# Performance work log

Measured on AMD Instinct MI355X. Metric: run time of the kernel, lower is better.

## Reference

```python
import jax, jax.numpy as jnp
import numpy as np

E = 8           # num experts
T = 8192        # total tokens
K = 4096        # input dim
N = 4096        # output dim


def setup_inputs() -> dict:
    key = jax.random.key(0)
    k1, k2, k3 = jax.random.split(key, 3)
    a = jax.random.normal(k1, (T, K), dtype=jnp.float32)
    b = jax.random.normal(k2, (E, N, K), dtype=jnp.float32) * 0.02  # column-major expert weights
    c = jnp.zeros((T, N), dtype=jnp.float32)
    inner = jnp.sort(jax.random.randint(k3, (E - 1,), 0, T))
    seg_indptr = jnp.concatenate([jnp.zeros((1,), jnp.int64),
                                  inner.astype(jnp.int64),
                                  jnp.full((1,), T, jnp.int64)])
    weight_indices = jnp.arange(E, dtype=jnp.int64)
    return {"a": a, "b": b, "c": c, "seg_indptr": seg_indptr,
            "weight_indices": weight_indices, "batch_size": E}


def reference(a, b, c, seg_indptr, weight_indices, batch_size):
    # Grouped GEMM: tokens in segment [seg_indptr[e], seg_indptr[e+1]) use
    # expert weight b[weight_indices[e]] (column-major: out = a @ W.T).
    t = a.shape[0]
    b_sel = b[weight_indices]                                  # [E, N, K]
    out_all = jnp.einsum('tk,enk->etn', a, b_sel)              # [E, T, N]
    tok = jnp.arange(t)
    # expert id of each token from sorted segment boundaries
    eid = jnp.clip(jnp.searchsorted(seg_indptr, tok, side='right') - 1,
                   0, batch_size - 1)
    return out_all[eid, tok]                                   # [T, N]
```

## Files before the change

kernel.cpp:

```cpp
#include <hip/hip_runtime.h>
#include <hip/hip_bf16.h>

typedef float f32x4 __attribute__((ext_vector_type(4)));
typedef short bf16x8 __attribute__((ext_vector_type(8)));
typedef unsigned short u16;

constexpr int T_TOK = 8192;
constexpr int KDIM  = 4096;
constexpr int NDIM  = 4096;
constexpr int NE    = 8;

constexpr long long TA = (long long)T_TOK * KDIM;
constexpr long long TB = (long long)NE * NDIM * KDIM;

__device__ __forceinline__ u16 f2bf(float f) {
  unsigned u = __builtin_bit_cast(unsigned, f);
  u += 0x7FFFu + ((u >> 16) & 1u);
  return (u16)(u >> 16);
}

__global__ __launch_bounds__(256)
void cvt_bf16(const float* __restrict__ A, const float* __restrict__ B,
              u16* __restrict__ oA, u16* __restrict__ oB) {
  const long long nv = (TA + TB) >> 3;
  const long long stride = (long long)gridDim.x * blockDim.x;
  for (long long i = (long long)blockIdx.x * blockDim.x + threadIdx.x; i < nv; i += stride) {
    const long long e = i << 3;
    const float* s;
    u16* d;
    if (e < TA) { s = A + e;        d = oA + e; }
    else        { s = B + (e - TA); d = oB + (e - TA); }
    f32x4 v0 = ((const f32x4*)s)[0];
    f32x4 v1 = ((const f32x4*)s)[1];
    bf16x8 p;
    #pragma unroll
    for (int j = 0; j < 4; ++j) p[j]     = (short)f2bf(v0[j]);
    #pragma unroll
    for (int j = 0; j < 4; ++j) p[4 + j] = (short)f2bf(v1[j]);
    *(bf16x8*)d = p;
  }
}

__device__ __forceinline__ void gload16(const u16* g, const u16* l) {
  __builtin_amdgcn_global_load_lds(
      (const __attribute__((address_space(1))) void*)g,
      (__attribute__((address_space(3))) void*)l, 16, 0, 0);
}

constexpr int BM2 = 256, BN2 = 256, BK2 = 64;
constexpr int NKT2 = KDIM / BK2;
constexpr int NTN2 = NDIM / BN2;
constexpr int MT2  = T_TOK / BM2 + NE;
constexpr int NWG2 = MT2 * NTN2;
constexpr int ASZ  = BM2 * BK2;
constexpr int HSZ  = ASZ / 2;

__global__ __launch_bounds__(512, 2)
void gg8(const u16* __restrict__ Abf, const u16* __restrict__ Bbf,
         float* __restrict__ C, const int* __restrict__ segp,
         const int* __restrict__ widx)
{
  extern __shared__ u16 sm[];
  u16* sA = sm;
  u16* sB = sm + 2 * ASZ;

  int bid = (int)blockIdx.x;
  bid = (bid & 7) * (NWG2 / 8) + (bid >> 3);
  const int nt = bid % NTN2;
  const int mt = bid / NTN2;

  int e = -1, segs = 0, sege = 0, mloc = 0;
  {
    int acc0 = 0, sp = segp[0];
    #pragma unroll
    for (int i = 0; i < NE; ++i) {
      int sn = segp[i + 1];
      int nti = (sn - sp + BM2 - 1) / BM2;
      if (e < 0 && mt < acc0 + nti) { e = i; mloc = mt - acc0; segs = sp; sege = sn; }
      acc0 += nti; sp = sn;
    }
  }
  if (e < 0) return;

  const int row_base = segs + mloc * BM2;
  const int col_base = nt * BN2;
  const u16* __restrict__ W = Bbf + (long long)widx[e] * ((long long)NDIM * KDIM);

  const int tid = threadIdx.x, lane = tid & 63, wid = tid >> 6;
  const int wr = wid >> 2, wc = wid & 3;

  const int sg = (((lane & 7) ^ (lane >> 3)) << 3);
  const int rr = wid * 8 + (lane >> 3);
  int oA[2][2], oB[2][2];
  #pragma unroll
  for (int h = 0; h < 2; ++h)
    #pragma unroll
    for (int i = 0; i < 2; ++i) {
      oA[h][i] = min(row_base + h * 128 + i * 64 + rr, T_TOK - 1) * KDIM + sg;
      oB[h][i] = (col_base + h * 128 + i * 64 + rr) * KDIM + sg;
    }

  const int g0  = (lane >> 4) ^ (lane & 7);
  const int g1  = g0 ^ 4;
  const int rA0 = (wr * 64 + (lane & 15)) * BK2 + g0 * 8;
  const int rA1 = (wr * 64 + (lane & 15)) * BK2 + g1 * 8;
  const int rB0 = (wc * 32 + (lane & 15)) * BK2 + g0 * 8;
  const int rB1 = (wc * 32 + (lane & 15)) * BK2 + g1 * 8;

  f32x4 acc[8][4];
  #pragma unroll
  for (int m = 0; m < 8; ++m)
    #pragma unroll
    for (int n = 0; n < 4; ++n)
      acc[m][n] = (f32x4){0.f, 0.f, 0.f, 0.f};

  bf16x8 aF[4][2], bF0[2][2], bF1[2][2];

  auto STGA = [&](int bbuf, int h, int t) __attribute__((always_inline)) {
    gload16(Abf + oA[h][0] + t * BK2, sA + bbuf * ASZ + h * HSZ + wid * 512);
    gload16(Abf + oA[h][1] + t * BK2, sA + bbuf * ASZ + h * HSZ + 4096 + wid * 512);
  };
  auto STGB = [&](int bbuf, int h, int t) __attribute__((always_inline)) {
    gload16(W + oB[h][0] + t * BK2, sB + bbuf * ASZ + h * HSZ + wid * 512);
    gload16(W + oB[h][1] + t * BK2, sB + bbuf * ASZ + h * HSZ + 4096 + wid * 512);
  };
  auto LDA = [&](int bbuf, int mh) __attribute__((always_inline)) {
    #pragma unroll
    for (int j = 0; j < 4; ++j) {
      const u16* p = sA + bbuf * ASZ + mh * HSZ + j * 16 * BK2;
      aF[j][0] = *(const bf16x8*)(p + rA0);
      aF[j][1] = *(const bf16x8*)(p + rA1);
    }
  };
  auto LDB = [&](int bbuf, int nh, bf16x8 (&bF)[2][2]) __attribute__((always_inline)) {
    #pragma unroll
    for (int i = 0; i < 2; ++i) {
      const u16* p = sB + bbuf * ASZ + nh * HSZ + i * 16 * BK2;
      bF[i][0] = *(const bf16x8*)(p + rB0);
      bF[i][1] = *(const bf16x8*)(p + rB1);
    }
  };
  auto MF = [&](int mh, int nh, bf16x8 (&bF)[2][2]) __attribute__((always_inline)) {
    __builtin_amdgcn_s_setprio(1);
    #pragma unroll
    for (int j = 0; j < 4; ++j)
      #pragma unroll
      for (int i = 0; i < 2; ++i) {
        acc[mh * 4 + j][nh * 2 + i] = __builtin_amdgcn_mfma_f32_16x16x32_bf16(
            aF[j][0], bF[i][0], acc[mh * 4 + j][nh * 2 + i], 0, 0, 0);
        acc[mh * 4 + j][nh * 2 + i] = __builtin_amdgcn_mfma_f32_16x16x32_bf16(
            aF[j][1], bF[i][1], acc[mh * 4 + j][nh * 2 + i], 0, 0, 0);
      }
    __builtin_amdgcn_s_setprio(0);
  };

  STGA(0, 0, 0); STGB(0, 0, 0); STGA(0, 1, 0); STGB(0, 1, 0);
  STGA(1, 0, 1); STGB(1, 0, 1);
  asm volatile("s_waitcnt vmcnt(4)" ::: "memory");
  __builtin_amdgcn_s_barrier();

  for (int t = 0; t < NKT2; ++t) {
    const int bb = t & 1, nb = bb ^ 1;

    LDA(bb, 0); LDB(bb, 0, bF0); LDB(bb, 1, bF1);
    if (t + 1 < NKT2) { STGA(nb, 1, t + 1); STGB(nb, 1, t + 1); }
    MF(0, 0, bF0); MF(0, 1, bF1);
    __builtin_amdgcn_s_barrier();

    LDA(bb, 1);
    if (t + 2 < NKT2) { STGA(bb, 0, t + 2); STGB(bb, 0, t + 2); }
    MF(1, 0, bF0); MF(1, 1, bF1);
    if (t + 2 < NKT2) {
      asm volatile("s_waitcnt vmcnt(4)" ::: "memory");
    } else {
      asm volatile("s_waitcnt vmcnt(0)" ::: "memory");
    }
    __builtin_amdgcn_s_barrier();
  }

  #pragma unroll
  for (int m = 0; m < 8; ++m) {
    const int r0 = row_base + (m >> 2) * 128 + wr * 64 + (m & 3) * 16 + ((lane >> 4) << 2);
    #pragma unroll
    for (int j = 0; j < 4; ++j) {
      const int r = r0 + j;
      if (r < sege) {
        float* cp = C + (long long)r * NDIM + col_base + (lane & 15);
        #pragma unroll
        for (int n = 0; n < 4; ++n)
          cp[(n >> 1) * 128 + wc * 32 + (n & 1) * 16] = acc[m][n][j];
      }
    }
  }
}

constexpr int BM = 128, BN = 128, BK = 32;
constexpr int LDKF = BK + 8;
constexpr int NTN = NDIM / BN;
constexpr int MT_MAX = T_TOK / BM + NE;
constexpr int NKT = KDIM / BK;
constexpr int NWG = MT_MAX * NTN;

__global__ __launch_bounds__(256, 2)
void grouped_gemm_fused(const float* __restrict__ A, const float* __restrict__ B,
                        float* __restrict__ C, const int* __restrict__ segp,
                        const int* __restrict__ widx)
{
  __shared__ u16 lA[2][BM][LDKF];
  __shared__ u16 lB[2][BN][LDKF];

  const int nt = blockIdx.x % NTN;
  const int mt = blockIdx.x / NTN;

  int e = -1, segs = 0, sege = 0, mloc = 0;
  {
    int acc0 = 0, sp = segp[0];
    #pragma unroll
    for (int i = 0; i < NE; ++i) {
      int sn = segp[i + 1];
      int nti = (sn - sp + BM - 1) / BM;
      if (e < 0 && mt < acc0 + nti) { e = i; mloc = mt - acc0; segs = sp; sege = sn; }
      acc0 += nti; sp = sn;
    }
  }
  if (e < 0) return;

  const int row_base = segs + mloc * BM;
  const int col_base = nt * BN;
  const float* __restrict__ W = B + (long long)widx[e] * NDIM * KDIM;

  const int tid  = threadIdx.x;
  const int lane = tid & 63;
  const int wid  = tid >> 6;
  const int wr   = wid >> 1;
  const int wc   = wid & 1;

  const int srow = tid >> 1;
  const int scol = (tid & 1) << 4;
  const int arow = min(row_base + srow, T_TOK - 1);
  const float* __restrict__ aptr = A + (long long)arow * KDIM + scol;
  const float* __restrict__ bptr = W + (long long)(col_base + srow) * KDIM + scol;

  f32x4 sa[4], sb[4];
  f32x4 acc[4][4];
  #pragma unroll
  for (int m = 0; m < 4; ++m)
    #pragma unroll
    for (int n = 0; n < 4; ++n)
      acc[m][n] = (f32x4){0.f, 0.f, 0.f, 0.f};

  const int frow = lane & 15;
  const int fk   = (lane >> 4) << 3;

  auto load_tiles = [&](int kt) {
    const float* ap = aptr + kt * BK;
    const float* bp = bptr + kt * BK;
    #pragma unroll
    for (int i = 0; i < 4; ++i) sa[i] = *(const f32x4*)(ap + i * 4);
    #pragma unroll
    for (int i = 0; i < 4; ++i) sb[i] = *(const f32x4*)(bp + i * 4);
  };
  auto conv_write = [&](int buf) {
    u16* wa = &lA[buf][srow][scol];
    u16* wb = &lB[buf][srow][scol];
    bf16x8 p;
    #pragma unroll
    for (int j = 0; j < 8; ++j) p[j] = (short)f2bf(sa[j >> 2][j & 3]);
    *(bf16x8*)(wa) = p;
    #pragma unroll
    for (int j = 0; j < 8; ++j) p[j] = (short)f2bf(sa[2 + (j >> 2)][j & 3]);
    *(bf16x8*)(wa + 8) = p;
    #pragma unroll
    for (int j = 0; j < 8; ++j) p[j] = (short)f2bf(sb[j >> 2][j & 3]);
    *(bf16x8*)(wb) = p;
    #pragma unroll
    for (int j = 0; j < 8; ++j) p[j] = (short)f2bf(sb[2 + (j >> 2)][j & 3]);
    *(bf16x8*)(wb + 8) = p;
  };

  load_tiles(0);
  conv_write(0);
  __syncthreads();

  int cur = 0;
  for (int kt = 0; kt < NKT; ++kt) {
    const bool more = (kt + 1 < NKT);
    if (more) load_tiles(kt + 1);

    bf16x8 af[4], bfr[4];
    #pragma unroll
    for (int m = 0; m < 4; ++m)
      af[m] = *(const bf16x8*)&lA[cur][wr * 64 + m * 16 + frow][fk];
    #pragma unroll
    for (int n = 0; n < 4; ++n)
      bfr[n] = *(const bf16x8*)&lB[cur][wc * 64 + n * 16 + frow][fk];

    if (more) conv_write(cur ^ 1);

    #pragma unroll
    for (int m = 0; m < 4; ++m)
      #pragma unroll
      for (int n = 0; n < 4; ++n)
        acc[m][n] = __builtin_amdgcn_mfma_f32_16x16x32_bf16(af[m], bfr[n], acc[m][n], 0, 0, 0);

    __syncthreads();
    cur ^= 1;
  }

  const int crow0 = row_base + wr * 64;
  const int ccol  = col_base + wc * 64 + (lane & 15);
  const int rsub  = (lane >> 4) << 2;
  #pragma unroll
  for (int m = 0; m < 4; ++m) {
    #pragma unroll
    for (int j = 0; j < 4; ++j) {
      const int r = crow0 + m * 16 + rsub + j;
      if (r < sege) {
        #pragma unroll
        for (int n = 0; n < 4; ++n)
          C[(long long)r * NDIM + ccol + n * 16] = acc[m][n][j];
      }
    }
  }
}

extern "C" void kernel_launch(void* const* d_in, const int* in_sizes, int n_in,
                              void* d_out, int out_size, void* d_ws, size_t ws_size,
                              hipStream_t stream) {
  const float* A   = (const float*)d_in[0];
  const float* B   = (const float*)d_in[1];
  const int* segp  = (const int*)d_in[3];
  const int* widx  = (const int*)d_in[4];
  float* C = (float*)d_out;

  const size_t need = (size_t)(TA + TB) * sizeof(u16);
  if (ws_size >= need) {
    u16* oA = (u16*)d_ws;
    u16* oB = oA + TA;
    cvt_bf16<<<dim3(2048), dim3(256), 0, stream>>>(A, B, oA, oB);
    (void)hipFuncSetAttribute((const void*)gg8,
                              hipFuncAttributeMaxDynamicSharedMemorySize,
                              2 * 2 * ASZ * (int)sizeof(u16));
    gg8<<<dim3(NWG2), dim3(512), 2 * 2 * ASZ * sizeof(u16), stream>>>(oA, oB, C, segp, widx);
  } else {
    grouped_gemm_fused<<<dim3(NWG), dim3(256), 0, stream>>>(A, B, C, segp, widx);
  }
}
```

Baseline: 492.1 us.

## Shrink bf16 grouped GEMM tile to 128x256x32 and simplify the pipeline

Replaces the 256x256x64 tile with a 128x256 tile and BK=32, and launch bounds now ask for 4 workgroups per CU instead of 2. The split-half LDS staging and interleaved MFMA schedule is replaced by a simpler loop: read all fragments, barrier, issue the next stage, then run 16 MFMAs. Per-workgroup LDS and registers drop, which should raise occupancy and cut padding waste on the last tile of each expert segment. In exchange, arithmetic intensity per tile is lower, there are more K iterations with barriers, and global traffic per flop rises.

```diff
diff --git a/kernel.cpp b/kernel.cpp
--- a/kernel.cpp
+++ b/kernel.cpp
@@ -47,27 +47,28 @@
       (__attribute__((address_space(3))) void*)l, 16, 0, 0);
 }
 
-constexpr int BM2 = 256, BN2 = 256, BK2 = 64;
-constexpr int NKT2 = KDIM / BK2;
-constexpr int NTN2 = NDIM / BN2;
-constexpr int MT2  = T_TOK / BM2 + NE;
-constexpr int NWG2 = MT2 * NTN2;
-constexpr int ASZ  = BM2 * BK2;
-constexpr int HSZ  = ASZ / 2;
-
-__global__ __launch_bounds__(512, 2)
+constexpr int BM3 = 128, BN3 = 256, BK3 = 32;
+constexpr int NKT3 = KDIM / BK3;
+constexpr int NTN3 = NDIM / BN3;
+constexpr int MT3  = T_TOK / BM3 + NE;
+constexpr int NWG3 = MT3 * NTN3;
+constexpr int ASZA = BM3 * BK3;
+constexpr int ASZB = BN3 * BK3;
+constexpr int LDS_BYTES = 2 * (ASZA + ASZB) * (int)sizeof(u16);
+
+__global__ __launch_bounds__(512, 4)
 void gg8(const u16* __restrict__ Abf, const u16* __restrict__ Bbf,
          float* __restrict__ C, const int* __restrict__ segp,
          const int* __restrict__ widx)
 {
   extern __shared__ u16 sm[];
   u16* sA = sm;
-  u16* sB = sm + 2 * ASZ;
+  u16* sB = sm + 2 * ASZA;
 
   int bid = (int)blockIdx.x;
-  bid = (bid & 7) * (NWG2 / 8) + (bid >> 3);
-  const int nt = bid % NTN2;
-  const int mt = bid / NTN2;
+  bid = (bid & 7) * (NWG3 / 8) + (bid >> 3);
+  const int nt = bid % NTN3;
+  const int mt = bid / NTN3;
 
   int e = -1, segs = 0, sege = 0, mloc = 0;
   {
@@ -75,103 +76,76 @@
     #pragma unroll
     for (int i = 0; i < NE; ++i) {
       int sn = segp[i + 1];
-      int nti = (sn - sp + BM2 - 1) / BM2;
+      int nti = (sn - sp + BM3 - 1) / BM3;
       if (e < 0 && mt < acc0 + nti) { e = i; mloc = mt - acc0; segs = sp; sege = sn; }
       acc0 += nti; sp = sn;
     }
   }
   if (e < 0) return;
 
-  const int row_base = segs + mloc * BM2;
-  const int col_base = nt * BN2;
+  const int row_base = segs + mloc * BM3;
+  const int col_base = nt * BN3;
   const u16* __restrict__ W = Bbf + (long long)widx[e] * ((long long)NDIM * KDIM);
 
   const int tid = threadIdx.x, lane = tid & 63, wid = tid >> 6;
   const int wr = wid >> 2, wc = wid & 3;
 
-  const int sg = (((lane & 7) ^ (lane >> 3)) << 3);
-  const int rr = wid * 8 + (lane >> 3);
-  int oA[2][2], oB[2][2];
+  const int sgc = ((lane & 3) ^ ((lane >> 3) & 3)) * 8;
+  int oA, oB0, oB1;
+  {
+    const int ra = row_base + wid * 16 + (lane >> 2);
+    oA  = min(ra, T_TOK - 1) * KDIM + sgc;
+    oB0 = (col_base + wid * 32 +      (lane >> 2)) * KDIM + sgc;
+    oB1 = (col_base + wid * 32 + 16 + (lane >> 2)) * KDIM + sgc;
+  }
+
+  const int gp  = ((lane >> 4) ^ ((lane >> 1) & 3)) * 8;
+  const int rA0 = (wr * 64 + (lane & 15)) * BK3 + gp;
+  const int rB0 = (wc * 64 + (lane & 15)) * BK3 + gp;
+
+  f32x4 acc[4][4];
   #pragma unroll
-  for (int h = 0; h < 2; ++h)
-    #pragma unroll
-    for (int i = 0; i < 2; ++i) {
-      oA[h][i] = min(row_base + h * 128 + i * 64 + rr, T_TOK - 1) * KDIM + sg;
-      oB[h][i] = (col_base + h * 128 + i * 64 + rr) * KDIM + sg;
-    }
-
-  const int g0  = (lane >> 4) ^ (lane & 7);
-  const int g1  = g0 ^ 4;
-  const int rA0 = (wr * 64 + (lane & 15)) * BK2 + g0 * 8;
-  const int rA1 = (wr * 64 + (lane & 15)) * BK2 + g1 * 8;
-  const int rB0 = (wc * 32 + (lane & 15)) * BK2 + g0 * 8;
-  const int rB1 = (wc * 32 + (lane & 15)) * BK2 + g1 * 8;
-
-  f32x4 acc[8][4];
-  #pragma unroll
-  for (int m = 0; m < 8; ++m)
+  for (int m = 0; m < 4; ++m)
     #pragma unroll
     for (int n = 0; n < 4; ++n)
       acc[m][n] = (f32x4){0.f, 0.f, 0.f, 0.f};
 
-  bf16x8 aF[4][2], bF0[2][2], bF1[2][2];
-
-  auto STGA = [&](int bbuf, int h, int t) __attribute__((always_inline)) {
-    gload16(Abf + oA[h][0] + t * BK2, sA + bbuf * ASZ + h * HSZ + wid * 512);
-    gload16(Abf + oA[h][1] + t * BK2, sA + bbuf * ASZ + h * HSZ + 4096 + wid * 512);
+  auto STAGE = [&](int bbuf, int t) __attribute__((always_inline)) {
+    gload16(Abf + oA  + t * BK3, sA + bbuf * ASZA + wid * 512);
+    gload16(W   + oB0 + t * BK3, sB + bbuf * ASZB + wid * 1024);
+    gload16(W   + oB1 + t * BK3, sB + bbuf * ASZB + wid * 1024 + 512);
   };
-  auto STGB = [&](int bbuf, int h, int t) __attribute__((always_inline)) {
-    gload16(W + oB[h][0] + t * BK2, sB + bbuf * ASZ + h * HSZ + wid * 512);
-    gload16(W + oB[h][1] + t * BK2, sB + bbuf * ASZ + h * HSZ + 4096 + wid * 512);
-  };
-  auto LDA = [&](int bbuf, int mh) __attribute__((always_inline)) {
-    #pragma unroll
-    for (int j = 0; j < 4; ++j) {
-      const u16* p = sA + bbuf * ASZ + mh * HSZ + j * 16 * BK2;
-      aF[j][0] = *(const bf16x8*)(p + rA0);
-      aF[j][1] = *(const bf16x8*)(p + rA1);
-    }
-  };
-  auto LDB = [&](int bbuf, int nh, bf16x8 (&bF)[2][2]) __attribute__((always_inline)) {
-    #pragma unroll
-    for (int i = 0; i < 2; ++i) {
-      const u16* p = sB + bbuf * ASZ + nh * HSZ + i * 16 * BK2;
-      bF[i][0] = *(const bf16x8*)(p + rB0);
-      bF[i][1] = *(const bf16x8*)(p + rB1);
-    }
-  };
-  auto MF = [&](int mh, int nh, bf16x8 (&bF)[2][2]) __attribute__((always_inline)) {
+
+  STAGE(0, 0); STAGE(1, 1);
+  asm volatile("s_waitcnt vmcnt(3)" ::: "memory");
+  __builtin_amdgcn_s_barrier();
+
+  for (int t = 0; t < NKT3; ++t) {
+    const int bb = t & 1;
+
+    bf16x8 aF[4], bF[4];
+    #pragma unroll
+    for (int m = 0; m < 4; ++m)
+      aF[m] = *(const bf16x8*)(sA + bb * ASZA + rA0 + m * 512);
+    #pragma unroll
+    for (int n = 0; n < 4; ++n)
+      bF[n] = *(const bf16x8*)(sB + bb * ASZB + rB0 + n * 512);
+
+    asm volatile("s_waitcnt lgkmcnt(0)" ::: "memory");
+    __builtin_amdgcn_s_barrier();
+
+    if (t + 2 < NKT3) STAGE(bb, t + 2);
+
     __builtin_amdgcn_s_setprio(1);
     #pragma unroll
-    for (int j = 0; j < 4; ++j)
+    for (int m = 0; m < 4; ++m)
       #pragma unroll
-      for (int i = 0; i < 2; ++i) {
-        acc[mh * 4 + j][nh * 2 + i] = __builtin_amdgcn_mfma_f32_16x16x32_bf16(
-            aF[j][0], bF[i][0], acc[mh * 4 + j][nh * 2 + i], 0, 0, 0);
-        acc[mh * 4 + j][nh * 2 + i] = __builtin_amdgcn_mfma_f32_16x16x32_bf16(
-            aF[j][1], bF[i][1], acc[mh * 4 + j][nh * 2 + i], 0, 0, 0);
-      }
+      for (int n = 0; n < 4; ++n)
+        acc[m][n] = __builtin_amdgcn_mfma_f32_16x16x32_bf16(aF[m], bF[n], acc[m][n], 0, 0, 0);
     __builtin_amdgcn_s_setprio(0);
-  };
-
-  STGA(0, 0, 0); STGB(0, 0, 0); STGA(0, 1, 0); STGB(0, 1, 0);
-  STGA(1, 0, 1); STGB(1, 0, 1);
-  asm volatile("s_waitcnt vmcnt(4)" ::: "memory");
-  __builtin_amdgcn_s_barrier();
-
-  for (int t = 0; t < NKT2; ++t) {
-    const int bb = t & 1, nb = bb ^ 1;
-
-    LDA(bb, 0); LDB(bb, 0, bF0); LDB(bb, 1, bF1);
-    if (t + 1 < NKT2) { STGA(nb, 1, t + 1); STGB(nb, 1, t + 1); }
-    MF(0, 0, bF0); MF(0, 1, bF1);
-    __builtin_amdgcn_s_barrier();
-
-    LDA(bb, 1);
-    if (t + 2 < NKT2) { STGA(bb, 0, t + 2); STGB(bb, 0, t + 2); }
-    MF(1, 0, bF0); MF(1, 1, bF1);
-    if (t + 2 < NKT2) {
-      asm volatile("s_waitcnt vmcnt(4)" ::: "memory");
+
+    if (t + 2 < NKT3) {
+      asm volatile("s_waitcnt vmcnt(3)" ::: "memory");
     } else {
       asm volatile("s_waitcnt vmcnt(0)" ::: "memory");
     }
@@ -179,16 +153,16 @@
   }
 
   #pragma unroll
-  for (int m = 0; m < 8; ++m) {
-    const int r0 = row_base + (m >> 2) * 128 + wr * 64 + (m & 3) * 16 + ((lane >> 4) << 2);
+  for (int m = 0; m < 4; ++m) {
+    const int r0 = row_base + wr * 64 + m * 16 + ((lane >> 4) << 2);
     #pragma unroll
     for (int j = 0; j < 4; ++j) {
       const int r = r0 + j;
       if (r < sege) {
-        float* cp = C + (long long)r * NDIM + col_base + (lane & 15);
+        float* cp = C + (long long)r * NDIM + col_base + wc * 64 + (lane & 15);
         #pragma unroll
         for (int n = 0; n < 4; ++n)
-          cp[(n >> 1) * 128 + wc * 32 + (n & 1) * 16] = acc[m][n][j];
+          cp[n * 16] = acc[m][n][j];
       }
     }
   }
@@ -340,8 +314,8 @@
     cvt_bf16<<<dim3(2048), dim3(256), 0, stream>>>(A, B, oA, oB);
     (void)hipFuncSetAttribute((const void*)gg8,
                               hipFuncAttributeMaxDynamicSharedMemorySize,
-                              2 * 2 * ASZ * (int)sizeof(u16));
-    gg8<<<dim3(NWG2), dim3(512), 2 * 2 * ASZ * sizeof(u16), stream>>>(oA, oB, C, segp, widx);
+                              LDS_BYTES);
+    gg8<<<dim3(NWG3), dim3(512), LDS_BYTES, stream>>>(oA, oB, C, segp, widx);
   } else {
     grouped_gemm_fused<<<dim3(NWG), dim3(256), 0, stream>>>(A, B, C, segp, widx);
   }
```

Measured after the change: 568.2 us. +15.5%, slower.

## Switch grouped GEMM inner loop to 32x32x16 bf16 MFMA with new LDS swizzle

Applied to the files above, without the earlier changes.

Replaces the 16x16x32 MFMA tiling with 32x32x16 MFMA instructions. Each wave now owns a 64-column strip made of two 32x32 fragments in N and two in M per half. The LDS write swizzle gains an extra XOR by wave index, and the read pattern changes to match the 32-lane fragment layout. The aim is fewer LDS fragment reads per FLOP and higher MFMA throughput per instruction. In exchange it rewrites the epilogue mapping and risks bank conflicts or a mismatch between the write and read swizzles.

```diff
diff --git a/kernel.cpp b/kernel.cpp
--- a/kernel.cpp
+++ b/kernel.cpp
@@ -2,6 +2,7 @@
 #include <hip/hip_bf16.h>
 
 typedef float f32x4 __attribute__((ext_vector_type(4)));
+typedef float f32x16 __attribute__((ext_vector_type(16)));
 typedef short bf16x8 __attribute__((ext_vector_type(8)));
 typedef unsigned short u16;
 
@@ -89,7 +90,7 @@
   const int tid = threadIdx.x, lane = tid & 63, wid = tid >> 6;
   const int wr = wid >> 2, wc = wid & 3;
 
-  const int sg = (((lane & 7) ^ (lane >> 3)) << 3);
+  const int sg = (((lane & 7) ^ ((lane >> 3) & 7) ^ (wid & 3)) << 3);
   const int rr = wid * 8 + (lane >> 3);
   int oA[2][2], oB[2][2];
   #pragma unroll
@@ -100,21 +101,23 @@
       oB[h][i] = (col_base + h * 128 + i * 64 + rr) * KDIM + sg;
     }
 
-  const int g0  = (lane >> 4) ^ (lane & 7);
-  const int g1  = g0 ^ 4;
-  const int rA0 = (wr * 64 + (lane & 15)) * BK2 + g0 * 8;
-  const int rA1 = (wr * 64 + (lane & 15)) * BK2 + g1 * 8;
-  const int rB0 = (wc * 32 + (lane & 15)) * BK2 + g0 * 8;
-  const int rB1 = (wc * 32 + (lane & 15)) * BK2 + g1 * 8;
-
-  f32x4 acc[8][4];
-  #pragma unroll
-  for (int m = 0; m < 8; ++m)
-    #pragma unroll
-    for (int n = 0; n < 4; ++n)
-      acc[m][n] = (f32x4){0.f, 0.f, 0.f, 0.f};
-
-  bf16x8 aF[4][2], bF0[2][2], bF1[2][2];
+  const int klane = (lane & 7) ^ ((lane >> 3) & 3);
+  int pgk[4];
+  #pragma unroll
+  for (int ks = 0; ks < 4; ++ks)
+    pgk[ks] = ((ks * 2 + (lane >> 5)) ^ klane) * 8;
+  const int rAin = (wr * 64 + (lane & 31)) * BK2;
+  const int rBin = ((wc & 1) * 64 + (lane & 31)) * BK2;
+  const int hB   = wc >> 1;
+
+  f32x16 acc[2][2][2];
+  #pragma unroll
+  for (int a = 0; a < 2; ++a)
+    #pragma unroll
+    for (int b = 0; b < 2; ++b)
+      #pragma unroll
+      for (int c = 0; c < 2; ++c)
+        acc[a][b][c] = (f32x16)(0.f);
 
   auto STGA = [&](int bbuf, int h, int t) __attribute__((always_inline)) {
     gload16(Abf + oA[h][0] + t * BK2, sA + bbuf * ASZ + h * HSZ + wid * 512);
@@ -124,52 +127,55 @@
     gload16(W + oB[h][0] + t * BK2, sB + bbuf * ASZ + h * HSZ + wid * 512);
     gload16(W + oB[h][1] + t * BK2, sB + bbuf * ASZ + h * HSZ + 4096 + wid * 512);
   };
-  auto LDA = [&](int bbuf, int mh) __attribute__((always_inline)) {
-    #pragma unroll
-    for (int j = 0; j < 4; ++j) {
-      const u16* p = sA + bbuf * ASZ + mh * HSZ + j * 16 * BK2;
-      aF[j][0] = *(const bf16x8*)(p + rA0);
-      aF[j][1] = *(const bf16x8*)(p + rA1);
-    }
-  };
-  auto LDB = [&](int bbuf, int nh, bf16x8 (&bF)[2][2]) __attribute__((always_inline)) {
-    #pragma unroll
-    for (int i = 0; i < 2; ++i) {
-      const u16* p = sB + bbuf * ASZ + nh * HSZ + i * 16 * BK2;
-      bF[i][0] = *(const bf16x8*)(p + rB0);
-      bF[i][1] = *(const bf16x8*)(p + rB1);
-    }
-  };
-  auto MF = [&](int mh, int nh, bf16x8 (&bF)[2][2]) __attribute__((always_inline)) {
-    __builtin_amdgcn_s_setprio(1);
-    #pragma unroll
-    for (int j = 0; j < 4; ++j)
-      #pragma unroll
-      for (int i = 0; i < 2; ++i) {
-        acc[mh * 4 + j][nh * 2 + i] = __builtin_amdgcn_mfma_f32_16x16x32_bf16(
-            aF[j][0], bF[i][0], acc[mh * 4 + j][nh * 2 + i], 0, 0, 0);
-        acc[mh * 4 + j][nh * 2 + i] = __builtin_amdgcn_mfma_f32_16x16x32_bf16(
-            aF[j][1], bF[i][1], acc[mh * 4 + j][nh * 2 + i], 0, 0, 0);
-      }
-    __builtin_amdgcn_s_setprio(0);
-  };
 
   STGA(0, 0, 0); STGB(0, 0, 0); STGA(0, 1, 0); STGB(0, 1, 0);
   STGA(1, 0, 1); STGB(1, 0, 1);
   asm volatile("s_waitcnt vmcnt(4)" ::: "memory");
   __builtin_amdgcn_s_barrier();
 
+  bf16x8 aF[2][4], bF[2][4];
   for (int t = 0; t < NKT2; ++t) {
     const int bb = t & 1, nb = bb ^ 1;
 
-    LDA(bb, 0); LDB(bb, 0, bF0); LDB(bb, 1, bF1);
+    #pragma unroll
+    for (int nf = 0; nf < 2; ++nf)
+      #pragma unroll
+      for (int ks = 0; ks < 4; ++ks)
+        bF[nf][ks] = *(const bf16x8*)(sB + bb * ASZ + hB * HSZ + rBin + nf * 2048 + pgk[ks]);
+    #pragma unroll
+    for (int mf = 0; mf < 2; ++mf)
+      #pragma unroll
+      for (int ks = 0; ks < 4; ++ks)
+        aF[mf][ks] = *(const bf16x8*)(sA + bb * ASZ + rAin + mf * 2048 + pgk[ks]);
     if (t + 1 < NKT2) { STGA(nb, 1, t + 1); STGB(nb, 1, t + 1); }
-    MF(0, 0, bF0); MF(0, 1, bF1);
+    __builtin_amdgcn_s_setprio(1);
+    #pragma unroll
+    for (int ks = 0; ks < 4; ++ks)
+      #pragma unroll
+      for (int mf = 0; mf < 2; ++mf)
+        #pragma unroll
+        for (int nf = 0; nf < 2; ++nf)
+          acc[0][mf][nf] = __builtin_amdgcn_mfma_f32_32x32x16_bf16(
+              aF[mf][ks], bF[nf][ks], acc[0][mf][nf], 0, 0, 0);
+    __builtin_amdgcn_s_setprio(0);
     __builtin_amdgcn_s_barrier();
 
-    LDA(bb, 1);
+    #pragma unroll
+    for (int mf = 0; mf < 2; ++mf)
+      #pragma unroll
+      for (int ks = 0; ks < 4; ++ks)
+        aF[mf][ks] = *(const bf16x8*)(sA + bb * ASZ + HSZ + rAin + mf * 2048 + pgk[ks]);
     if (t + 2 < NKT2) { STGA(bb, 0, t + 2); STGB(bb, 0, t + 2); }
-    MF(1, 0, bF0); MF(1, 1, bF1);
+    __builtin_amdgcn_s_setprio(1);
+    #pragma unroll
+    for (int ks = 0; ks < 4; ++ks)
+      #pragma unroll
+      for (int mf = 0; mf < 2; ++mf)
+        #pragma unroll
+        for (int nf = 0; nf < 2; ++nf)
+          acc[1][mf][nf] = __builtin_amdgcn_mfma_f32_32x32x16_bf16(
+              aF[mf][ks], bF[nf][ks], acc[1][mf][nf], 0, 0, 0);
+    __builtin_amdgcn_s_setprio(0);
     if (t + 2 < NKT2) {
       asm volatile("s_waitcnt vmcnt(4)" ::: "memory");
     } else {
@@ -178,20 +184,24 @@
     __builtin_amdgcn_s_barrier();
   }
 
-  #pragma unroll
-  for (int m = 0; m < 8; ++m) {
-    const int r0 = row_base + (m >> 2) * 128 + wr * 64 + (m & 3) * 16 + ((lane >> 4) << 2);
-    #pragma unroll
-    for (int j = 0; j < 4; ++j) {
-      const int r = r0 + j;
-      if (r < sege) {
-        float* cp = C + (long long)r * NDIM + col_base + (lane & 15);
+  const int ccol = col_base + wc * 64 + (lane & 31);
+  #pragma unroll
+  for (int mh = 0; mh < 2; ++mh)
+    #pragma unroll
+    for (int mf = 0; mf < 2; ++mf) {
+      const int r0 = row_base + mh * 128 + wr * 64 + mf * 32 + ((lane >> 5) << 2);
+      #pragma unroll
+      for (int rq = 0; rq < 4; ++rq)
         #pragma unroll
-        for (int n = 0; n < 4; ++n)
-          cp[(n >> 1) * 128 + wc * 32 + (n & 1) * 16] = acc[m][n][j];
-      }
-    }
-  }
+        for (int rj = 0; rj < 4; ++rj) {
+          const int r = r0 + rq * 8 + rj;
+          if (r < sege) {
+            float* cp = C + (long long)r * NDIM + ccol;
+            cp[0]  = acc[mh][mf][0][rq * 4 + rj];
+            cp[32] = acc[mh][mf][1][rq * 4 + rj];
+          }
+        }
+    }
 }
 
 constexpr int BM = 128, BN = 128, BK = 32;
```

After: 539.1 us. +9.5%, slower.

## Split grouped GEMM into full-tile wave plus half-height tail kernel

Applied to the files above, without the earlier changes.

The first 512 256x256 tiles (one full wave at two workgroups per CU) now run in the original kernel. The remaining tail tiles go to a new kernel that splits each tile into two 128x256 halves, so twice as many workgroups share the tail work across CUs. The goal is to shrink the underfilled last wave and the imbalance it causes. The cost is a second kernel launch with a serialization point between the two, lower per-block reuse in the half tiles, and possibly wasted work on half tiles that fall past a segment end. Tile decoding is factored into a shared helper.

```diff
diff --git a/kernel.cpp b/kernel.cpp
--- a/kernel.cpp
+++ b/kernel.cpp
@@ -51,9 +51,24 @@
 constexpr int NKT2 = KDIM / BK2;
 constexpr int NTN2 = NDIM / BN2;
 constexpr int MT2  = T_TOK / BM2 + NE;
-constexpr int NWG2 = MT2 * NTN2;
+constexpr int NWG_TOT = MT2 * NTN2;
+constexpr int NWG_L1  = 512;
 constexpr int ASZ  = BM2 * BK2;
 constexpr int HSZ  = ASZ / 2;
+
+__device__ __forceinline__ bool decode_tile(const int* segp, int mt,
+                                            int& e, int& segs, int& sege, int& mloc) {
+  e = -1;
+  int acc0 = 0, sp = segp[0];
+  #pragma unroll
+  for (int i = 0; i < NE; ++i) {
+    int sn = segp[i + 1];
+    int nti = (sn - sp + BM2 - 1) / BM2;
+    if (e < 0 && mt < acc0 + nti) { e = i; mloc = mt - acc0; segs = sp; sege = sn; }
+    acc0 += nti; sp = sn;
+  }
+  return e >= 0;
+}
 
 __global__ __launch_bounds__(512, 2)
 void gg8(const u16* __restrict__ Abf, const u16* __restrict__ Bbf,
@@ -65,22 +80,12 @@
   u16* sB = sm + 2 * ASZ;
 
   int bid = (int)blockIdx.x;
-  bid = (bid & 7) * (NWG2 / 8) + (bid >> 3);
+  bid = (bid & 7) * (NWG_L1 / 8) + (bid >> 3);
   const int nt = bid % NTN2;
   const int mt = bid / NTN2;
 
-  int e = -1, segs = 0, sege = 0, mloc = 0;
-  {
-    int acc0 = 0, sp = segp[0];
-    #pragma unroll
-    for (int i = 0; i < NE; ++i) {
-      int sn = segp[i + 1];
-      int nti = (sn - sp + BM2 - 1) / BM2;
-      if (e < 0 && mt < acc0 + nti) { e = i; mloc = mt - acc0; segs = sp; sege = sn; }
-      acc0 += nti; sp = sn;
-    }
-  }
-  if (e < 0) return;
+  int e, segs, sege, mloc;
+  if (!decode_tile(segp, mt, e, segs, sege, mloc)) return;
 
   const int row_base = segs + mloc * BM2;
   const int col_base = nt * BN2;
@@ -194,6 +199,124 @@
   }
 }
 
+__global__ __launch_bounds__(512, 2)
+void gg_half(const u16* __restrict__ Abf, const u16* __restrict__ Bbf,
+             float* __restrict__ C, const int* __restrict__ segp,
+             const int* __restrict__ widx)
+{
+  extern __shared__ u16 sm[];
+  u16* sA = sm;
+  u16* sB = sm + 2 * HSZ;
+
+  int b = (int)blockIdx.x;
+  const int swz = (b & 7) * 32 + (b >> 3);
+  const int tile = NWG_L1 + (swz >> 1);
+  const int mh   = swz & 1;
+  const int nt = tile % NTN2;
+  const int mt = tile / NTN2;
+
+  int e, segs, sege, mloc;
+  if (!decode_tile(segp, mt, e, segs, sege, mloc)) return;
+
+  const int row_base = segs + mloc * BM2 + mh * 128;
+  const int col_base = nt * BN2;
+  const u16* __restrict__ W = Bbf + (long long)widx[e] * ((long long)NDIM * KDIM);
+
+  const int tid = threadIdx.x, lane = tid & 63, wid = tid >> 6;
+  const int wr = wid >> 2, wc = wid & 3;
+
+  const int sg = (((lane & 7) ^ (lane >> 3)) << 3);
+  const int rr = wid * 8 + (lane >> 3);
+  int oA[2], oB[4];
+  #pragma unroll
+  for (int i = 0; i < 2; ++i)
+    oA[i] = min(row_base + i * 64 + rr, T_TOK - 1) * KDIM + sg;
+  #pragma unroll
+  for (int i = 0; i < 4; ++i)
+    oB[i] = (col_base + i * 64 + rr) * KDIM + sg;
+
+  const int g0  = (lane >> 4) ^ (lane & 7);
+  const int g1  = g0 ^ 4;
+  const int rA0 = (wr * 64 + (lane & 15)) * BK2 + g0 * 8;
+  const int rA1 = (wr * 64 + (lane & 15)) * BK2 + g1 * 8;
+  const int rB0 = (wc * 64 + (lane & 15)) * BK2 + g0 * 8;
+  const int rB1 = (wc * 64 + (lane & 15)) * BK2 + g1 * 8;
+
+  f32x4 acc[4][4];
+  #pragma unroll
+  for (int m = 0; m < 4; ++m)
+    #pragma unroll
+    for (int n = 0; n < 4; ++n)
+      acc[m][n] = (f32x4){0.f, 0.f, 0.f, 0.f};
+
+  auto STAGE = [&](int bbuf, int t) __attribute__((always_inline)) {
+    gload16(Abf + oA[0] + t * BK2, sA + bbuf * HSZ + wid * 512);
+    gload16(Abf + oA[1] + t * BK2, sA + bbuf * HSZ + 4096 + wid * 512);
+    #pragma unroll
+    for (int i = 0; i < 4; ++i)
+      gload16(W + oB[i] + t * BK2, sB + bbuf * ASZ + i * 4096 + wid * 512);
+  };
+
+  STAGE(0, 0); STAGE(1, 1);
+  asm volatile("s_waitcnt vmcnt(6)" ::: "memory");
+  __builtin_amdgcn_s_barrier();
+
+  for (int t = 0; t < NKT2; ++t) {
+    const int bb = t & 1;
+
+    bf16x8 aF[4][2], bF[4][2];
+    #pragma unroll
+    for (int m = 0; m < 4; ++m) {
+      const u16* p = sA + bb * HSZ + m * 16 * BK2;
+      aF[m][0] = *(const bf16x8*)(p + rA0);
+      aF[m][1] = *(const bf16x8*)(p + rA1);
+    }
+    #pragma unroll
+    for (int n = 0; n < 4; ++n) {
+      const u16* p = sB + bb * ASZ + n * 16 * BK2;
+      bF[n][0] = *(const bf16x8*)(p + rB0);
+      bF[n][1] = *(const bf16x8*)(p + rB1);
+    }
+
+    asm volatile("s_waitcnt lgkmcnt(0)" ::: "memory");
+    __builtin_amdgcn_s_barrier();
+
+    if (t + 2 < NKT2) STAGE(bb, t + 2);
+
+    __builtin_amdgcn_s_setprio(1);
+    #pragma unroll
+    for (int m = 0; m < 4; ++m)
+      #pragma unroll
+      for (int n = 0; n < 4; ++n) {
+        acc[m][n] = __builtin_amdgcn_mfma_f32_16x16x32_bf16(aF[m][0], bF[n][0], acc[m][n], 0, 0, 0);
+        acc[m][n] = __builtin_amdgcn_mfma_f32_16x16x32_bf16(aF[m][1], bF[n][1], acc[m][n], 0, 0, 0);
+      }
+    __builtin_amdgcn_s_setprio(0);
+
+    if (t + 2 < NKT2) {
+      asm volatile("s_waitcnt vmcnt(6)" ::: "memory");
+    } else {
+      asm volatile("s_waitcnt vmcnt(0)" ::: "memory");
+    }
+    __builtin_amdgcn_s_barrier();
+  }
+
+  #pragma unroll
+  for (int m = 0; m < 4; ++m) {
+    const int r0 = row_base + wr * 64 + m * 16 + ((lane >> 4) << 2);
+    #pragma unroll
+    for (int j = 0; j < 4; ++j) {
+      const int r = r0 + j;
+      if (r < sege) {
+        float* cp = C + (long long)r * NDIM + col_base + wc * 64 + (lane & 15);
+        #pragma unroll
+        for (int n = 0; n < 4; ++n)
+          cp[n * 16] = acc[m][n][j];
+      }
+    }
+  }
+}
+
 constexpr int BM = 128, BN = 128, BK = 32;
 constexpr int LDKF = BK + 8;
 constexpr int NTN = NDIM / BN;
@@ -341,7 +464,12 @@
     (void)hipFuncSetAttribute((const void*)gg8,
                               hipFuncAttributeMaxDynamicSharedMemorySize,
                               2 * 2 * ASZ * (int)sizeof(u16));
-    gg8<<<dim3(NWG2), dim3(512), 2 * 2 * ASZ * sizeof(u16), stream>>>(oA, oB, C, segp, widx);
+    gg8<<<dim3(NWG_L1), dim3(512), 2 * 2 * ASZ * sizeof(u16), stream>>>(oA, oB, C, segp, widx);
+    (void)hipFuncSetAttribute((const void*)gg_half,
+                              hipFuncAttributeMaxDynamicSharedMemorySize,
+                              2 * (HSZ + ASZ) * (int)sizeof(u16));
+    gg_half<<<dim3((NWG_TOT - NWG_L1) * 2), dim3(512),
+              2 * (HSZ + ASZ) * sizeof(u16), stream>>>(oA, oB, C, segp, widx);
   } else {
     grouped_gemm_fused<<<dim3(NWG), dim3(256), 0, stream>>>(A, B, C, segp, widx);
   }
```

Result: no change. 484.5 us (-1.5%).
